# Kernel optimization log

Hardware: AMD Instinct MI355X
Metric: run time of the kernel (lower is better)

Reference implementation:

```python
import jax, jax.numpy as jnp
import numpy as np

N_NODES = 100000
N_EDGES = 1600000
IN_C, HID_C, OUT_C = 128, 256, 128


def setup_inputs() -> dict:
    key = jax.random.key(0)
    ks = jax.random.split(key, 6)
    x = jax.random.normal(ks[0], (N_NODES, IN_C), dtype=jnp.float32)
    edge_index = jax.random.randint(ks[1], (2, N_EDGES), 0, N_NODES, dtype=jnp.int64)
    s = 0.05
    W1a = jax.random.normal(ks[2], (IN_C, HID_C), dtype=jnp.float32) * s
    b1a = jnp.zeros((HID_C,), dtype=jnp.float32)
    W2a = jax.random.normal(ks[3], (HID_C, HID_C), dtype=jnp.float32) * s
    b2a = jnp.zeros((HID_C,), dtype=jnp.float32)
    W1b = jax.random.normal(ks[4], (HID_C, HID_C), dtype=jnp.float32) * s
    b1b = jnp.zeros((HID_C,), dtype=jnp.float32)
    W2b = jax.random.normal(ks[5], (HID_C, OUT_C), dtype=jnp.float32) * s
    b2b = jnp.zeros((OUT_C,), dtype=jnp.float32)
    return {"x": x, "edge_index": edge_index, "W1a": W1a, "b1a": b1a,
            "W2a": W2a, "b2a": b2a, "W1b": W1b, "b1b": b1b,
            "W2b": W2b, "b2b": b2b}


def _gin_conv(x, src, dst, W1, b1, W2, b2):
    # GINConv (eps=0): nn( x + sum_{j in N(i)} x_j )
    agg = jax.ops.segment_sum(x[src], dst, num_segments=N_NODES)  # [N, d]
    h = x + agg
    h = jnp.maximum(h @ W1 + b1, 0.0)
    return h @ W2 + b2


def reference(x, edge_index, W1a, b1a, W2a, b2a, W1b, b1b, W2b, b2b):
    src, dst = edge_index[0], edge_index[1]
    h = jnp.maximum(_gin_conv(x, src, dst, W1a, b1a, W2a, b2a), 0.0)  # relu(conv1)
    # dropout is identity in eval mode
    out = _gin_conv(h, src, dst, W1b, b1b, W2b, b2b)  # conv2
    return out
```

## Files before the change

### kernel.cpp

```cpp
#include <hip/hip_runtime.h>


#define N_NODES 100000
#define N_EDGES 1600000
#define NBUCK 13

typedef unsigned short ushort_t;
typedef short bf16x8 __attribute__((ext_vector_type(8)));
typedef float floatx4 __attribute__((ext_vector_type(4)));

static __device__ __forceinline__ ushort_t f2bf(float f) {
    unsigned u = __float_as_uint(f);
    u = (u + 0x7FFFu + ((u >> 16) & 1u)) >> 16;
    return (ushort_t)u;
}
static __device__ __forceinline__ unsigned pack2bf(float lo, float hi) {
    return (unsigned)f2bf(lo) | ((unsigned)f2bf(hi) << 16);
}
static __device__ __forceinline__ void addu4(float* acc, const uint4 v) {
    const unsigned w0 = v.x, w1 = v.y, w2 = v.z, w3 = v.w;
    acc[0] += __uint_as_float(w0 << 16);
    acc[1] += __uint_as_float(w0 & 0xFFFF0000u);
    acc[2] += __uint_as_float(w1 << 16);
    acc[3] += __uint_as_float(w1 & 0xFFFF0000u);
    acc[4] += __uint_as_float(w2 << 16);
    acc[5] += __uint_as_float(w2 & 0xFFFF0000u);
    acc[6] += __uint_as_float(w3 << 16);
    acc[7] += __uint_as_float(w3 & 0xFFFF0000u);
}

#define GLOAD_LDS16(g, l)                                                     \
    __builtin_amdgcn_global_load_lds(                                         \
        (const __attribute__((address_space(1))) void*)(g),                   \
        (__attribute__((address_space(3))) void*)(l), 16, 0, 0)

__global__ __launch_bounds__(256) void cvt_x_kernel(const float* __restrict__ X,
                                                    ushort_t* __restrict__ Xb, int n8) {
    int i = blockIdx.x * 256 + threadIdx.x;
    if (i < n8) {
        const float4 a = ((const float4*)X)[2 * i];
        const float4 b = ((const float4*)X)[2 * i + 1];
        uint4 r;
        r.x = pack2bf(a.x, a.y);
        r.y = pack2bf(a.z, a.w);
        r.z = pack2bf(b.x, b.y);
        r.w = pack2bf(b.z, b.w);
        ((uint4*)Xb)[i] = r;
    }
}

__global__ __launch_bounds__(256) void cvt_all_kernel(
    const float* __restrict__ W1a, const float* __restrict__ W2a,
    const float* __restrict__ W1b, const float* __restrict__ W2b,
    ushort_t* __restrict__ wt1a, ushort_t* __restrict__ wt2a,
    ushort_t* __restrict__ wt1b, ushort_t* __restrict__ wt2b) {
    int i = blockIdx.x * 256 + threadIdx.x;
    if (i < 32768) {
        int k = i >> 8, n = i & 255;
        wt1a[n * 128 + k] = f2bf(W1a[i]);
    } else if (i < 98304) {
        int j = i - 32768, k = j >> 8, n = j & 255;
        wt2a[n * 256 + k] = f2bf(W2a[j]);
    } else if (i < 163840) {
        int j = i - 98304, k = j >> 8, n = j & 255;
        wt1b[n * 256 + k] = f2bf(W1b[j]);
    } else if (i < 196608) {
        int j = i - 163840, k = j >> 7, n = j & 127;
        wt2b[n * 256 + k] = f2bf(W2b[j]);
    }
}

__global__ __launch_bounds__(256) void hist_kernel(const int* __restrict__ src,
                                                   const int* __restrict__ dst,
                                                   int* __restrict__ deg, int nE) {
    const int bucket = blockIdx.y;
    for (int e = blockIdx.x * 256 + threadIdx.x; e < nE; e += gridDim.x * 256) {
        int d = dst[e];
        int s = src[e];
        if ((unsigned)d < (unsigned)N_NODES && (unsigned)s < (unsigned)N_NODES &&
            (d >> 13) == bucket)
            atomicAdd(&deg[d], 1);
    }
}

__global__ __launch_bounds__(256) void fill_kernel(const int* __restrict__ src,
                                                   const int* __restrict__ dst,
                                                   int* __restrict__ cursor,
                                                   int* __restrict__ csr_src, int nE) {
    const int bucket = blockIdx.y;
    for (int e = blockIdx.x * 256 + threadIdx.x; e < nE; e += gridDim.x * 256) {
        int d = dst[e];
        int s = src[e];
        if ((unsigned)d < (unsigned)N_NODES && (unsigned)s < (unsigned)N_NODES &&
            (d >> 13) == bucket) {
            int pos = atomicAdd(&cursor[d], 1);
            csr_src[pos] = s;
        }
    }
}

__global__ __launch_bounds__(256) void scan1_kernel(const int* __restrict__ deg,
                                                    int* __restrict__ bsum, int n) {
    __shared__ int l[256];
    int b = blockIdx.x, t = threadIdx.x;
    int base = b * 1024 + t * 4;
    int s = 0;
#pragma unroll
    for (int k = 0; k < 4; ++k) {
        int i = base + k;
        if (i < n) s += deg[i];
    }
    l[t] = s;
    __syncthreads();
    for (int off = 128; off > 0; off >>= 1) {
        if (t < off) l[t] += l[t + off];
        __syncthreads();
    }
    if (t == 0) bsum[b] = l[0];
}

__global__ __launch_bounds__(128) void scan2_kernel(const int* __restrict__ bsum,
                                                    int* __restrict__ boff, int nb) {
    __shared__ int l[128];
    int t = threadIdx.x;
    int v = (t < nb) ? bsum[t] : 0;
    l[t] = v;
    __syncthreads();
    for (int off = 1; off < 128; off <<= 1) {
        int add = (t >= off) ? l[t - off] : 0;
        __syncthreads();
        l[t] += add;
        __syncthreads();
    }
    if (t < nb) boff[t] = l[t] - v;
}

__global__ __launch_bounds__(256) void scan3_kernel(const int* __restrict__ deg,
                                                    const int* __restrict__ boff,
                                                    int* __restrict__ row_ptr,
                                                    int* __restrict__ cursor, int n) {
    __shared__ int l[256];
    int b = blockIdx.x, t = threadIdx.x;
    int base = b * 1024 + t * 4;
    int d[4];
    int s = 0;
#pragma unroll
    for (int k = 0; k < 4; ++k) {
        int i = base + k;
        d[k] = (i < n) ? deg[i] : 0;
        s += d[k];
    }
    l[t] = s;
    __syncthreads();
    for (int off = 1; off < 256; off <<= 1) {
        int add = (t >= off) ? l[t - off] : 0;
        __syncthreads();
        l[t] += add;
        __syncthreads();
    }
    int run = boff[b] + l[t] - s;
#pragma unroll
    for (int k = 0; k < 4; ++k) {
        int i = base + k;
        if (i < n) {
            row_ptr[i] = run;
            cursor[i] = run;
        }
        run += d[k];
    }
}

template <int C, int U>
__global__ __launch_bounds__(256) void agg_gather_kernel(
    const ushort_t* __restrict__ X, ushort_t* __restrict__ T,
    const int* __restrict__ row_ptr, const int* __restrict__ deg,
    const int* __restrict__ csr_src, const ushort_t* __restrict__ zrow, int nN) {
    constexpr int G = C / 8;
    constexpr int NPW = 64 / G;
    constexpr int B = U * NPW;
    const int lane = threadIdx.x & 63;
    const int wid = threadIdx.x >> 6;
    const int node = blockIdx.x * 4 + wid;
    if (node >= nN) return;
    const int sub = lane / G;
    const int coff = (lane % G) * 8;

    float acc[8];
#pragma unroll
    for (int k = 0; k < 8; ++k) acc[k] = 0.f;

    const int base = row_ptr[node];
    const int dg = deg[node];
    for (int j0 = 0; j0 < dg; j0 += 64) {
        int cnt = dg - j0;
        if (cnt > 64) cnt = 64;
        int nidx = (lane < cnt) ? csr_src[base + j0 + lane] : 0;
        if ((unsigned)nidx >= (unsigned)N_NODES) nidx = 0;
        for (int j = 0; j < cnt; j += B) {
            uint4 v[U];
#pragma unroll
            for (int u = 0; u < U; ++u) {
                int jj = j + u * NPW + sub;
                bool ok = jj < cnt;
                int idx = __shfl(nidx, ok ? jj : 0);
                const ushort_t* p = ok ? (X + (size_t)idx * C) : zrow;
                v[u] = *(const uint4*)(p + coff);
            }
#pragma unroll
            for (int u = 0; u < U; ++u) addu4(acc, v[u]);
        }
    }
    if (sub == 0) {
        uint4 v = *(const uint4*)(X + (size_t)node * C + coff);
        addu4(acc, v);
    }
#pragma unroll
    for (int off = G; off < 64; off <<= 1)
#pragma unroll
        for (int k = 0; k < 8; ++k) acc[k] += __shfl_xor(acc[k], off);

    if (lane < G) {
        uint4 r;
        r.x = pack2bf(acc[0], acc[1]);
        r.y = pack2bf(acc[2], acc[3]);
        r.z = pack2bf(acc[4], acc[5]);
        r.w = pack2bf(acc[6], acc[7]);
        *(uint4*)(T + (size_t)node * C + coff) = r;
    }
}

template <bool RELU, typename OT>
__global__ __launch_bounds__(256) void gemm_kernel(
    const ushort_t* A, const ushort_t* __restrict__ Wt,
    const float* __restrict__ bias, OT* C, int M, int N, int K) {
    constexpr int BM = 128, BN = 128, BK = 32;
    __shared__ ushort_t As[BM * BK];
    __shared__ ushort_t Bs[BN * BK];

    const int tid = threadIdx.x;
    const int lane = tid & 63;
    const int wid = tid >> 6;
    const int wm = wid & 1;
    const int wn = wid >> 1;
    const int l15 = lane & 15;
    const int q = lane >> 4;
    const int srow = lane >> 2;
    const int scol = (lane & 3) * 8;

    const int bm = blockIdx.x * BM;
    const int bn = blockIdx.y * BN;

    floatx4 acc[4][4];
#pragma unroll
    for (int mi = 0; mi < 4; ++mi)
#pragma unroll
        for (int ni = 0; ni < 4; ++ni) {
            floatx4 z = {0.f, 0.f, 0.f, 0.f};
            acc[mi][ni] = z;
        }

    for (int kt = 0; kt < K; kt += BK) {
#pragma unroll
        for (int half = 0; half < 2; ++half) {
            const int row = wid * 32 + half * 16 + srow;
            const int gr = bm + row;
            const ushort_t* gpa = A + (size_t)gr * K + kt + scol;
            ushort_t* lpa = &As[(wid * 32 + half * 16) * BK];
            if (gr < M) GLOAD_LDS16(gpa, lpa);
            const ushort_t* gpb = Wt + (size_t)(bn + row) * K + kt + scol;
            ushort_t* lpb = &Bs[(wid * 32 + half * 16) * BK];
            GLOAD_LDS16(gpb, lpb);
        }
        __syncthreads();

        bf16x8 av[4], bv[4];
#pragma unroll
        for (int mi = 0; mi < 4; ++mi)
            av[mi] = *(const bf16x8*)&As[(wm * 64 + mi * 16 + l15) * BK + q * 8];
#pragma unroll
        for (int ni = 0; ni < 4; ++ni)
            bv[ni] = *(const bf16x8*)&Bs[(wn * 64 + ni * 16 + l15) * BK + q * 8];
#pragma unroll
        for (int mi = 0; mi < 4; ++mi)
#pragma unroll
            for (int ni = 0; ni < 4; ++ni)
                acc[mi][ni] = __builtin_amdgcn_mfma_f32_16x16x32_bf16(
                    av[mi], bv[ni], acc[mi][ni], 0, 0, 0);
        __syncthreads();
    }

    float bval[4];
#pragma unroll
    for (int ni = 0; ni < 4; ++ni) bval[ni] = bias[bn + wn * 64 + ni * 16 + l15];
#pragma unroll
    for (int mi = 0; mi < 4; ++mi) {
#pragma unroll
        for (int r = 0; r < 4; ++r) {
            int row = bm + wm * 64 + mi * 16 + q * 4 + r;
            if (row < M) {
#pragma unroll
                for (int ni = 0; ni < 4; ++ni) {
                    int col = bn + wn * 64 + ni * 16 + l15;
                    float v = acc[mi][ni][r] + bval[ni];
                    if (RELU) v = v > 0.f ? v : 0.f;
                    if constexpr (sizeof(OT) == 2)
                        C[(size_t)row * N + col] = f2bf(v);
                    else
                        C[(size_t)row * N + col] = v;
                }
            }
        }
    }
}

extern "C" void kernel_launch(void* const* d_in, const int* in_sizes, int n_in,
                              void* d_out, int out_size, void* d_ws, size_t ws_size,
                              hipStream_t stream) {
    const float* x   = (const float*)d_in[0];
    const int*   ei  = (const int*)d_in[1];
    const float* W1a = (const float*)d_in[2];
    const float* b1a = (const float*)d_in[3];
    const float* W2a = (const float*)d_in[4];
    const float* b2a = (const float*)d_in[5];
    const float* W1b = (const float*)d_in[6];
    const float* b1b = (const float*)d_in[7];
    const float* W2b = (const float*)d_in[8];
    const float* b2b = (const float*)d_in[9];
    const int* src = ei;
    const int* dst = ei + N_EDGES;
    float* out = (float*)d_out;

    char* base = (char*)d_ws;
    size_t o = 0;
    ushort_t* wt1a = (ushort_t*)(base + o); o += 128 * 256 * 2;
    ushort_t* wt2a = (ushort_t*)(base + o); o += 256 * 256 * 2;
    ushort_t* wt1b = (ushort_t*)(base + o); o += 256 * 256 * 2;
    ushort_t* wt2b = (ushort_t*)(base + o); o += 256 * 128 * 2;
    o = (o + 255) & ~(size_t)255;
    ushort_t* zrow = (ushort_t*)(base + o); o += 512;
    int* deg     = (int*)(base + o); o += (size_t)N_NODES * 4;
    int* row_ptr = (int*)(base + o); o += (size_t)N_NODES * 4;
    int* cursor  = (int*)(base + o); o += (size_t)N_NODES * 4;
    int* bsum    = (int*)(base + o); o += 128 * 4;
    int* boff    = (int*)(base + o); o += 128 * 4;
    o = (o + 255) & ~(size_t)255;
    int* csr_src = (int*)(base + o); o += (size_t)N_EDGES * 4;
    o = (o + 255) & ~(size_t)255;
    ushort_t* t1   = (ushort_t*)(base + o); o += (size_t)N_NODES * 128 * 2;
    ushort_t* tbig = (ushort_t*)(base + o); o += (size_t)N_NODES * 256 * 2;
    o += 128 * 1024;
    (void)ws_size; (void)o; (void)in_sizes; (void)n_in; (void)out_size;

    ushort_t* inter = (ushort_t*)d_out;
    ushort_t* xb    = (ushort_t*)d_out;

    cvt_all_kernel<<<768, 256, 0, stream>>>(W1a, W2a, W1b, W2b,
                                            wt1a, wt2a, wt1b, wt2b);
    cvt_x_kernel<<<(N_NODES * 128 / 8 + 255) / 256, 256, 0, stream>>>(
        x, xb, N_NODES * 128 / 8);

    const int NB = (N_NODES + 1023) / 1024;
    hipMemsetAsync(zrow, 0, 512 + (size_t)N_NODES * 4, stream);
    hist_kernel<<<dim3(1024, NBUCK), 256, 0, stream>>>(src, dst, deg, N_EDGES);
    scan1_kernel<<<NB, 256, 0, stream>>>(deg, bsum, N_NODES);
    scan2_kernel<<<1, 128, 0, stream>>>(bsum, boff, NB);
    scan3_kernel<<<NB, 256, 0, stream>>>(deg, boff, row_ptr, cursor, N_NODES);
    fill_kernel<<<dim3(1024, NBUCK), 256, 0, stream>>>(src, dst, cursor, csr_src,
                                                       N_EDGES);

    const int gm = (N_NODES + 127) / 128;
    const int ga = (N_NODES + 3) / 4;

    agg_gather_kernel<128, 4><<<ga, 256, 0, stream>>>(xb, t1, row_ptr, deg,
                                                      csr_src, zrow, N_NODES);
    gemm_kernel<true, ushort_t><<<dim3(gm, 2), 256, 0, stream>>>(
        t1, wt1a, b1a, tbig, N_NODES, 256, 128);
    gemm_kernel<true, ushort_t><<<dim3(gm, 2), 256, 0, stream>>>(
        tbig, wt2a, b2a, inter, N_NODES, 256, 256);

    agg_gather_kernel<256, 8><<<ga, 256, 0, stream>>>(inter, tbig, row_ptr,
                                                      deg, csr_src, zrow, N_NODES);
    gemm_kernel<true, ushort_t><<<dim3(gm, 2), 256, 0, stream>>>(
        tbig, wt1b, b1b, inter, N_NODES, 256, 256);
    gemm_kernel<false, float><<<dim3(gm, 1), 256, 0, stream>>>(
        inter, wt2b, b2b, out, N_NODES, 128, 256);
}
```

Measured before the change: 575.7 us.

## Fuse each GIN MLP's two GEMMs into one kernel with LDS intermediate

Replaces the pair of GEMM launches per GIN layer with a single mlp_kernel. It computes the hidden 256-wide activation for a 64-row tile, applies bias and ReLU, and stores it as bf16 in a swizzled LDS buffer. It then runs the second GEMM straight from LDS, so the hidden tensor never makes a round trip through global memory. The first GEMM is computed transposed (weights as the M operand), and each block now reloads both weight matrices per 64-row tile. The larger LDS footprint (about 48KB) may limit occupancy.

```diff
diff --git a/kernel.cpp b/kernel.cpp
--- a/kernel.cpp
+++ b/kernel.cpp
@@ -229,26 +229,25 @@
     }
 }
 
-template <bool RELU, typename OT>
-__global__ __launch_bounds__(256) void gemm_kernel(
-    const ushort_t* A, const ushort_t* __restrict__ Wt,
-    const float* __restrict__ bias, OT* C, int M, int N, int K) {
-    constexpr int BM = 128, BN = 128, BK = 32;
+template <int K1, int N2, bool RELU2, typename OT>
+__global__ __launch_bounds__(256, 3) void mlp_kernel(
+    const ushort_t* __restrict__ A, const ushort_t* __restrict__ Wt1,
+    const float* __restrict__ b1, const ushort_t* __restrict__ Wt2,
+    const float* __restrict__ b2, OT* __restrict__ C, int M) {
+    constexpr int N1 = 256, BM = 64, BK = 32;
+    constexpr int NPW2 = N2 / 4;
+    constexpr int RN2 = NPW2 / 16;
     __shared__ ushort_t As[BM * BK];
-    __shared__ ushort_t Bs[BN * BK];
-
-    const int tid = threadIdx.x;
-    const int lane = tid & 63;
-    const int wid = tid >> 6;
-    const int wm = wid & 1;
-    const int wn = wid >> 1;
+    __shared__ ushort_t Bs[N1 * BK];
+    __shared__ ushort_t U[BM * N1];
+
+    const int lane = threadIdx.x & 63;
+    const int wid = threadIdx.x >> 6;
     const int l15 = lane & 15;
     const int q = lane >> 4;
     const int srow = lane >> 2;
     const int scol = (lane & 3) * 8;
-
     const int bm = blockIdx.x * BM;
-    const int bn = blockIdx.y * BN;
 
     floatx4 acc[4][4];
 #pragma unroll
@@ -259,27 +258,25 @@
             acc[mi][ni] = z;
         }
 
-    for (int kt = 0; kt < K; kt += BK) {
-#pragma unroll
-        for (int half = 0; half < 2; ++half) {
-            const int row = wid * 32 + half * 16 + srow;
-            const int gr = bm + row;
-            const ushort_t* gpa = A + (size_t)gr * K + kt + scol;
-            ushort_t* lpa = &As[(wid * 32 + half * 16) * BK];
-            if (gr < M) GLOAD_LDS16(gpa, lpa);
-            const ushort_t* gpb = Wt + (size_t)(bn + row) * K + kt + scol;
-            ushort_t* lpb = &Bs[(wid * 32 + half * 16) * BK];
-            GLOAD_LDS16(gpb, lpb);
-        }
-        __syncthreads();
-
+    for (int kt = 0; kt < K1; kt += BK) {
+        {
+            const int gr = bm + wid * 16 + srow;
+            if (gr < M)
+                GLOAD_LDS16(A + (size_t)gr * K1 + kt + scol, &As[(wid * 16) * BK]);
+        }
+#pragma unroll
+        for (int u = 0; u < 4; ++u) {
+            const int row = wid * 64 + u * 16;
+            GLOAD_LDS16(Wt1 + (size_t)(row + srow) * K1 + kt + scol, &Bs[row * BK]);
+        }
+        __syncthreads();
         bf16x8 av[4], bv[4];
 #pragma unroll
         for (int mi = 0; mi < 4; ++mi)
-            av[mi] = *(const bf16x8*)&As[(wm * 64 + mi * 16 + l15) * BK + q * 8];
+            av[mi] = *(const bf16x8*)&Bs[(wid * 64 + mi * 16 + l15) * BK + q * 8];
 #pragma unroll
         for (int ni = 0; ni < 4; ++ni)
-            bv[ni] = *(const bf16x8*)&Bs[(wn * 64 + ni * 16 + l15) * BK + q * 8];
+            bv[ni] = *(const bf16x8*)&As[(ni * 16 + l15) * BK + q * 8];
 #pragma unroll
         for (int mi = 0; mi < 4; ++mi)
 #pragma unroll
@@ -289,24 +286,80 @@
         __syncthreads();
     }
 
-    float bval[4];
-#pragma unroll
-    for (int ni = 0; ni < 4; ++ni) bval[ni] = bias[bn + wn * 64 + ni * 16 + l15];
 #pragma unroll
     for (int mi = 0; mi < 4; ++mi) {
+        const int h0 = wid * 64 + mi * 16 + q * 4;
+        const float4 b4 = *(const float4*)&b1[h0];
+#pragma unroll
+        for (int ni = 0; ni < 4; ++ni) {
+            const int node = ni * 16 + l15;
+            float v0 = acc[mi][ni][0] + b4.x; v0 = v0 > 0.f ? v0 : 0.f;
+            float v1 = acc[mi][ni][1] + b4.y; v1 = v1 > 0.f ? v1 : 0.f;
+            float v2 = acc[mi][ni][2] + b4.z; v2 = v2 > 0.f ? v2 : 0.f;
+            float v3 = acc[mi][ni][3] + b4.w; v3 = v3 > 0.f ? v3 : 0.f;
+            uint2 w;
+            w.x = pack2bf(v0, v1);
+            w.y = pack2bf(v2, v3);
+            int byte = node * (N1 * 2) + h0 * 2;
+            byte ^= (node & 7) << 4;
+            *(uint2*)((char*)U + byte) = w;
+        }
+    }
+    __syncthreads();
+
+#pragma unroll
+    for (int mi = 0; mi < 4; ++mi)
+#pragma unroll
+        for (int ni = 0; ni < 4; ++ni) {
+            floatx4 z = {0.f, 0.f, 0.f, 0.f};
+            acc[mi][ni] = z;
+        }
+
+    for (int kt = 0; kt < N1; kt += BK) {
+#pragma unroll
+        for (int u = 0; u < RN2; ++u) {
+            const int row = wid * NPW2 + u * 16;
+            GLOAD_LDS16(Wt2 + (size_t)(row + srow) * N1 + kt + scol, &Bs[row * BK]);
+        }
+        __syncthreads();
+        bf16x8 av[4], bv[RN2];
+#pragma unroll
+        for (int mi = 0; mi < 4; ++mi) {
+            const int node = mi * 16 + l15;
+            const int byte =
+                (node * (N1 * 2) + kt * 2 + q * 16) ^ ((node & 7) << 4);
+            av[mi] = *(const bf16x8*)((const char*)U + byte);
+        }
+#pragma unroll
+        for (int ni = 0; ni < RN2; ++ni)
+            bv[ni] = *(const bf16x8*)&Bs[(wid * NPW2 + ni * 16 + l15) * BK + q * 8];
+#pragma unroll
+        for (int mi = 0; mi < 4; ++mi)
+#pragma unroll
+            for (int ni = 0; ni < RN2; ++ni)
+                acc[mi][ni] = __builtin_amdgcn_mfma_f32_16x16x32_bf16(
+                    av[mi], bv[ni], acc[mi][ni], 0, 0, 0);
+        __syncthreads();
+    }
+
+    float bval[RN2];
+#pragma unroll
+    for (int ni = 0; ni < RN2; ++ni) bval[ni] = b2[wid * NPW2 + ni * 16 + l15];
+#pragma unroll
+    for (int mi = 0; mi < 4; ++mi) {
 #pragma unroll
         for (int r = 0; r < 4; ++r) {
-            int row = bm + wm * 64 + mi * 16 + q * 4 + r;
+            const int row = bm + mi * 16 + q * 4 + r;
             if (row < M) {
 #pragma unroll
-                for (int ni = 0; ni < 4; ++ni) {
-                    int col = bn + wn * 64 + ni * 16 + l15;
+                for (int ni = 0; ni < RN2; ++ni) {
+                    const int col = wid * NPW2 + ni * 16 + l15;
                     float v = acc[mi][ni][r] + bval[ni];
-                    if (RELU) v = v > 0.f ? v : 0.f;
+                    if (RELU2) v = v > 0.f ? v : 0.f;
                     if constexpr (sizeof(OT) == 2)
-                        C[(size_t)row * N + col] = f2bf(v);
+                        C[(size_t)row * N2 + col] = f2bf(v);
                     else
-                        C[(size_t)row * N + col] = v;
+                        C[(size_t)row * N2 + col] = v;
                 }
             }
         }
@@ -368,20 +421,16 @@
     fill_kernel<<<dim3(1024, NBUCK), 256, 0, stream>>>(src, dst, cursor, csr_src,
                                                        N_EDGES);
 
-    const int gm = (N_NODES + 127) / 128;
     const int ga = (N_NODES + 3) / 4;
+    const int gf = (N_NODES + 63) / 64;
 
     agg_gather_kernel<128, 4><<<ga, 256, 0, stream>>>(xb, t1, row_ptr, deg,
                                                       csr_src, zrow, N_NODES);
-    gemm_kernel<true, ushort_t><<<dim3(gm, 2), 256, 0, stream>>>(
-        t1, wt1a, b1a, tbig, N_NODES, 256, 128);
-    gemm_kernel<true, ushort_t><<<dim3(gm, 2), 256, 0, stream>>>(
-        tbig, wt2a, b2a, inter, N_NODES, 256, 256);
+    mlp_kernel<128, 256, true, ushort_t><<<gf, 256, 0, stream>>>(
+        t1, wt1a, b1a, wt2a, b2a, inter, N_NODES);
 
     agg_gather_kernel<256, 8><<<ga, 256, 0, stream>>>(inter, tbig, row_ptr,
                                                       deg, csr_src, zrow, N_NODES);
-    gemm_kernel<true, ushort_t><<<dim3(gm, 2), 256, 0, stream>>>(
-        tbig, wt1b, b1b, inter, N_NODES, 256, 256);
-    gemm_kernel<false, float><<<dim3(gm, 1), 256, 0, stream>>>(
-        inter, wt2b, b2b, out, N_NODES, 128, 256);
-}
+    mlp_kernel<256, 128, false, float><<<gf, 256, 0, stream>>>(
+        tbig, wt1b, b1b, wt2b, b2b, out, N_NODES);
+}
```

Result: faster. 543.2 us (-5.6%).
